# Optimization experiments

Measured on AMD Instinct MI355X. Metric: run time of the kernel, lower is better.

## Reference

```python
import jax, jax.numpy as jnp
import numpy as np

N = 50000       # nodes
E = 800000      # edges (avg degree 16)
R = 8           # relations
IN = 128        # in_channels
H = 128         # hidden_size
B = 10          # graphs in batch
NPG = N // B    # nodes per graph (equal-size graphs)
NEG_SLOPE = 0.2 # RGATConv default negative_slope


def setup_inputs() -> dict:
    key = jax.random.key(0)
    ks = jax.random.split(key, 12)
    s = 0.1
    x = jax.random.normal(ks[0], (N, IN), dtype=jnp.float32)
    edge_index = jax.random.randint(ks[1], (2, E), 0, N, dtype=jnp.int32)
    edge_type = jax.random.randint(ks[2], (E,), 0, R, dtype=jnp.int32)
    batch = jnp.repeat(jnp.arange(B, dtype=jnp.int32), NPG)
    W1 = jax.random.normal(ks[3], (R, IN, H), dtype=jnp.float32) * s
    q1 = jax.random.normal(ks[4], (H, 1), dtype=jnp.float32) * s
    k1 = jax.random.normal(ks[5], (H, 1), dtype=jnp.float32) * s
    b1 = jnp.zeros((H,), dtype=jnp.float32)
    W2 = jax.random.normal(ks[6], (R, H, H), dtype=jnp.float32) * s
    q2 = jax.random.normal(ks[7], (H, 1), dtype=jnp.float32) * s
    k2 = jax.random.normal(ks[8], (H, 1), dtype=jnp.float32) * s
    b2 = jnp.zeros((H,), dtype=jnp.float32)
    Wl = jax.random.normal(ks[9], (H, H), dtype=jnp.float32) * s
    bl = jnp.zeros((H,), dtype=jnp.float32)
    return dict(x=x, edge_index=edge_index, edge_type=edge_type, batch=batch,
                W1=W1, q1=q1, k1=k1, b1=b1, W2=W2, q2=q2, k2=k2, b2=b2,
                Wl=Wl, bl=bl)


def _rgat_conv(x, src, tgt, etype, W, q, k, b):
    # Per-relation transform once per node ([R,N,H]), then gather per edge;
    # mathematically identical to PyG's per-edge bmm but avoids the [E,in,H] blowup.
    xW = jnp.einsum('ni,rio->rno', x, W)          # [R, N, H]
    outi = xW[etype, tgt]                          # [E, H] transformed target feats
    outj = xW[etype, src]                          # [E, H] transformed source feats
    # additive self-attention, heads=1, dim=1
    alpha = jax.nn.leaky_relu(outi @ q + outj @ k, NEG_SLOPE)  # [E, 1]
    # across-relation segment softmax over incoming edges of each target node
    m = jax.ops.segment_max(alpha, tgt, num_segments=N)        # [N, 1]
    a = jnp.exp(alpha - m[tgt])
    den = jax.ops.segment_sum(a, tgt, num_segments=N)          # [N, 1]
    a = a / (den[tgt] + 1e-16)
    out = jax.ops.segment_sum(a * outj, tgt, num_segments=N)   # [N, H]
    return out + b


def reference(x, edge_index, edge_type, batch, W1, q1, k1, b1,
              W2, q2, k2, b2, Wl, bl):
    src, tgt = edge_index[0], edge_index[1]
    h = jax.nn.relu(_rgat_conv(x, src, tgt, edge_type, W1, q1, k1, b1))
    # dropout p=0 -> identity
    h = jax.nn.relu(_rgat_conv(h, src, tgt, edge_type, W2, q2, k2, b2))
    h = h @ Wl.T + bl                               # nn.Linear
    # to_dense_batch: batch is sorted with equal-size graphs of NPG nodes
    return h.reshape(B, NPG, H)
```

## Files before the change

### kernel.cpp

```cpp
#include <hip/hip_runtime.h>


typedef unsigned int uint;
typedef unsigned short ushort_t;

using bf16x8 = __attribute__((ext_vector_type(8))) __bf16;
using f32x4  = __attribute__((ext_vector_type(4))) float;

__device__ __forceinline__ ushort_t fToBf(float f) {
  uint u = __float_as_uint(f);
  u += 0x7FFFu + ((u >> 16) & 1);
  return (ushort_t)(u >> 16);
}
__device__ __forceinline__ float bfToF(ushort_t h) {
  return __uint_as_float(((uint)h) << 16);
}
__device__ __forceinline__ uint packBf(float a, float b) {
  return (uint)fToBf(a) | ((uint)fToBf(b) << 16);
}


__global__ void k_count2(const int* __restrict__ tgt, const int* __restrict__ et,
                         int* __restrict__ deg2, int E) {
  int e = blockIdx.x * 256 + threadIdx.x;
  if (e < E) atomicAdd(&deg2[tgt[e] * 8 + et[e]], 1);
}

__global__ void k_scanA(const int* __restrict__ deg, int* __restrict__ incl,
                        int* __restrict__ bsum, int n) {
  __shared__ int s[256];
  int tid = threadIdx.x;
  int i = blockIdx.x * 256 + tid;
  int v = (i < n) ? deg[i] : 0;
  s[tid] = v;
  __syncthreads();
  for (int off = 1; off < 256; off <<= 1) {
    int t = (tid >= off) ? s[tid - off] : 0;
    __syncthreads();
    s[tid] += t;
    __syncthreads();
  }
  if (i < n) incl[i] = s[tid];
  if (tid == 255) bsum[blockIdx.x] = s[255];
}

__global__ void k_scanB2(int* __restrict__ bsum, int nb) {
  __shared__ int s[256];
  __shared__ int carry;
  int tid = threadIdx.x;
  if (tid == 0) carry = 0;
  __syncthreads();
  for (int base = 0; base < nb; base += 256) {
    int i = base + tid;
    int v = (i < nb) ? bsum[i] : 0;
    s[tid] = v;
    __syncthreads();
    for (int off = 1; off < 256; off <<= 1) {
      int t = (tid >= off) ? s[tid - off] : 0;
      __syncthreads();
      s[tid] += t;
      __syncthreads();
    }
    int c = carry;
    if (i < nb) bsum[i] = c + s[tid] - v;
    __syncthreads();
    if (tid == 255) carry = c + s[255];
    __syncthreads();
  }
}

__global__ void k_scanC(const int* __restrict__ deg, const int* __restrict__ incl,
                        const int* __restrict__ bsum, int* __restrict__ rowptr,
                        int n, int E) {
  int i = blockIdx.x * 256 + threadIdx.x;
  if (i < n) {
    rowptr[i] = bsum[blockIdx.x] + incl[i] - deg[i];
    if (i == n - 1) rowptr[n] = E;
  }
}

__global__ void k_scatter2(const int* __restrict__ src, const int* __restrict__ tgt,
                           const int* __restrict__ et, const int* __restrict__ rowptr2,
                           int* __restrict__ cursor2, int* __restrict__ sorted, int E) {
  int e = blockIdx.x * 256 + threadIdx.x;
  if (e >= E) return;
  int t8r = tgt[e] * 8 + et[e];
  int pos = atomicAdd(&cursor2[t8r], 1);
  sorted[rowptr2[t8r] + pos] = src[e] | (et[e] << 16);
}


__global__ void k_wsT(const float* __restrict__ W1, const float* __restrict__ W2,
                      ushort_t* __restrict__ WsT) {
  int idx = blockIdx.x * 256 + threadIdx.x;
  int n = idx & 127;
  int k = (idx >> 7) & 127;
  int rl = idx >> 14;
  const float* W = (rl >> 3) ? W2 : W1;
  int r = rl & 7;
  float v = W[((size_t)r * 128 + k) * 128 + n];
  WsT[((size_t)rl * 128 + n) * 128 + k] = fToBf(v);
}

__global__ void k_wqwk(const float* __restrict__ W1, const float* __restrict__ q1,
                       const float* __restrict__ k1, const float* __restrict__ W2,
                       const float* __restrict__ q2, const float* __restrict__ k2,
                       ushort_t* __restrict__ wqk) {
  int g = blockIdx.x * 256 + threadIdx.x;
  if (g >= 4096) return;
  int layer = g >> 11;
  int which = (g >> 10) & 1;
  int idx = g & 1023;
  const float* w = (layer ? W2 : W1) + (size_t)idx * 128;
  const float* v = layer ? (which ? k2 : q2) : (which ? k1 : q1);
  float s = 0.f;
  #pragma unroll 8
  for (int h = 0; h < 128; h++) s += w[h] * v[h];
  int r = idx >> 7, kin = idx & 127;
  wqk[(size_t)layer * 2048 + ((which << 3) + r) * 128 + kin] = fToBf(s);
}


template <bool F32IN>
__global__ __launch_bounds__(256) void
k_score(const void* __restrict__ Ain,
        const ushort_t* __restrict__ Wqk,
        ushort_t* __restrict__ xb,
        float* __restrict__ stbl,
        int M) {
  int tid = threadIdx.x, wv = tid >> 6, lane = tid & 63;
  int l15 = lane & 15, quad = lane >> 4;
  int node0 = blockIdx.x * 128 + wv * 32;

  bf16x8 bx[2][4];
  #pragma unroll
  for (int tile = 0; tile < 2; tile++) {
    int node = node0 + tile * 16 + l15;
    int nc = node < M ? node : M - 1;
    if (F32IN) {
      const float* row = (const float*)Ain + (size_t)nc * 128;
      #pragma unroll
      for (int kb = 0; kb < 4; kb++) {
        float4 a = *(const float4*)(row + kb * 32 + quad * 8);
        float4 b = *(const float4*)(row + kb * 32 + quad * 8 + 4);
        union { bf16x8 v; ushort_t u[8]; } t;
        t.u[0] = fToBf(a.x); t.u[1] = fToBf(a.y); t.u[2] = fToBf(a.z); t.u[3] = fToBf(a.w);
        t.u[4] = fToBf(b.x); t.u[5] = fToBf(b.y); t.u[6] = fToBf(b.z); t.u[7] = fToBf(b.w);
        bx[tile][kb] = t.v;
      }
    } else {
      const ushort_t* row = (const ushort_t*)Ain + (size_t)nc * 128;
      #pragma unroll
      for (int kb = 0; kb < 4; kb++)
        bx[tile][kb] = *(const bf16x8*)(row + kb * 32 + quad * 8);
    }
  }

  if (F32IN) {
    #pragma unroll
    for (int tile = 0; tile < 2; tile++) {
      int node = node0 + tile * 16 + l15;
      if (node < M) {
        #pragma unroll
        for (int kb = 0; kb < 4; kb++)
          *(bf16x8*)(xb + (size_t)node * 128 + kb * 32 + quad * 8) = bx[tile][kb];
      }
    }
  }

  bf16x8 aq[4];
  #pragma unroll
  for (int kb = 0; kb < 4; kb++)
    aq[kb] = *(const bf16x8*)(Wqk + (size_t)l15 * 128 + kb * 32 + quad * 8);
  #pragma unroll
  for (int tile = 0; tile < 2; tile++) {
    f32x4 s = {};
    #pragma unroll
    for (int kb = 0; kb < 4; kb++)
      s = __builtin_amdgcn_mfma_f32_16x16x32_bf16(aq[kb], bx[tile][kb], s, 0, 0, 0);
    int node = node0 + tile * 16 + l15;
    if (node < M) {
      float4 v = {s[0], s[1], s[2], s[3]};
      *(float4*)(stbl + (size_t)node * 16 + quad * 4) = v;
    }
  }
}


__global__ __launch_bounds__(256) void
k_gather(const ushort_t* __restrict__ feat,
         const float* __restrict__ stbl,
         const int* __restrict__ rp2,
         const int* __restrict__ sorted,
         ushort_t* __restrict__ g,
         int n) {
  __shared__ int   s_pk[4][64];
  __shared__ float s_al[4][64];
  __shared__ float s_w[4][64];
  int tid = threadIdx.x, wv = tid >> 6, lane = tid & 63;
  int t = blockIdx.x * 4 + wv;
  if (t >= n) return;
  int e0 = rp2[t * 8], e1 = rp2[t * 8 + 8];

  float m = -INFINITY, den = 0.f;
  for (int base = e0; base < e1; base += 64) {
    int cnt = min(64, e1 - base);
    float alpha = -INFINITY;
    if (lane < cnt) {
      int pk = sorted[base + lane];
      int s = pk & 0xFFFF, r = pk >> 16;
      float a = stbl[(size_t)t * 16 + r] + stbl[(size_t)s * 16 + 8 + r];
      alpha = (a >= 0.f) ? a : 0.2f * a;
      s_pk[wv][lane] = pk;
      s_al[wv][lane] = alpha;
    }
    float cm = alpha;
    #pragma unroll
    for (int off = 32; off; off >>= 1) cm = fmaxf(cm, __shfl_xor(cm, off, 64));
    float nm = fmaxf(m, cm);
    float w = (lane < cnt) ? __expf(alpha - nm) : 0.f;
    float ws = w;
    #pragma unroll
    for (int off = 32; off; off >>= 1) ws += __shfl_xor(ws, off, 64);
    den = den * __expf(m - nm) + ws;
    m = nm;
  }
  float inv = (den > 0.f) ? 1.f / (den + 1e-16f) : 0.f;

  const uint* fx = (const uint*)feat;
  uint* grow = (uint*)(g + (size_t)t * 1024);
  float ga = 0.f, gb = 0.f;
  int rw = 0;
  bool stored = (e1 - e0) <= 64;

  for (int base = e0; base < e1; base += 64) {
    int cnt = min(64, e1 - base);
    if (lane < cnt) {
      int pk; float a;
      if (stored) {
        pk = s_pk[wv][lane];
        a = s_al[wv][lane];
      } else {
        pk = sorted[base + lane];
        int s = pk & 0xFFFF, r = pk >> 16;
        a = stbl[(size_t)t * 16 + r] + stbl[(size_t)s * 16 + 8 + r];
        a = (a >= 0.f) ? a : 0.2f * a;
        s_pk[wv][lane] = pk;
      }
      s_w[wv][lane] = __expf(a - m) * inv;
    }
    for (int i = 0; i < cnt; i++) {
      int pk = s_pk[wv][i];
      float w = s_w[wv][i];
      int r = pk >> 16;
      if (r != rw) {
        grow[rw * 64 + lane] = packBf(ga, gb);
        for (int z = rw + 1; z < r; z++) grow[z * 64 + lane] = 0u;
        rw = r; ga = 0.f; gb = 0.f;
      }
      uint v = fx[(size_t)(pk & 0xFFFF) * 64 + lane];
      ga = __builtin_fmaf(w, bfToF((ushort_t)(v & 0xFFFF)), ga);
      gb = __builtin_fmaf(w, bfToF((ushort_t)(v >> 16)), gb);
    }
  }
  grow[rw * 64 + lane] = packBf(ga, gb);
  for (int z = rw + 1; z < 8; z++) grow[z * 64 + lane] = 0u;
}


#define LDA 136

__global__ __launch_bounds__(256) void
k_out(const ushort_t* __restrict__ g,
      const ushort_t* __restrict__ WsT,
      const float* __restrict__ bias,
      ushort_t* __restrict__ h,
      int M) {
  __shared__ ushort_t As[64 * LDA];
  __shared__ ushort_t Bs[128 * LDA];
  int tid = threadIdx.x, wv = tid >> 6, lane = tid & 63;
  int l15 = lane & 15, quad = lane >> 4;
  int row0 = blockIdx.x * 64;
  int wr = wv * 16;
  f32x4 acc[8] = {};

  for (int r = 0; r < 8; r++) {
    {
      int row = tid >> 2, seg = tid & 3;
      int4 z = {0, 0, 0, 0};
      int4 v0 = z, v1 = z, v2 = z, v3 = z;
      if (row0 + row < M) {
        const int4* src = (const int4*)(g + ((size_t)(row0 + row) * 8 + r) * 128 + seg * 32);
        v0 = src[0]; v1 = src[1]; v2 = src[2]; v3 = src[3];
      }
      int4* dst = (int4*)(As + row * LDA + seg * 32);
      dst[0] = v0; dst[1] = v1; dst[2] = v2; dst[3] = v3;
    }
    {
      const int4* src = (const int4*)(WsT + (size_t)r * 16384);
      for (int u = tid; u < 512; u += 256) {
        int rowb = u >> 2, seg = u & 3;
        int4* dst = (int4*)(Bs + rowb * LDA + seg * 32);
        #pragma unroll
        for (int j = 0; j < 4; j++) dst[j] = src[rowb * 16 + seg * 4 + j];
      }
    }
    __syncthreads();

    bf16x8 afr[4];
    #pragma unroll
    for (int kb = 0; kb < 4; kb++)
      afr[kb] = *(const bf16x8*)(As + (wr + l15) * LDA + kb * 32 + quad * 8);
    #pragma unroll
    for (int ct = 0; ct < 8; ct++)
      #pragma unroll
      for (int kb = 0; kb < 4; kb++) {
        bf16x8 bfr = *(const bf16x8*)(Bs + (ct * 16 + l15) * LDA + kb * 32 + quad * 8);
        acc[ct] = __builtin_amdgcn_mfma_f32_16x16x32_bf16(afr[kb], bfr, acc[ct], 0, 0, 0);
      }
    __syncthreads();
  }

  #pragma unroll
  for (int ct = 0; ct < 8; ct++) {
    float b = bias[ct * 16 + l15];
    #pragma unroll
    for (int reg = 0; reg < 4; reg++) {
      int rr = row0 + wr + quad * 4 + reg;
      if (rr < M)
        h[(size_t)rr * 128 + ct * 16 + l15] = fToBf(fmaxf(acc[ct][reg] + b, 0.f));
    }
  }
}


__global__ __launch_bounds__(256) void
k_gemmL(const ushort_t* __restrict__ A, const float* __restrict__ Wl,
        float* __restrict__ Cout, const float* __restrict__ bias, int M) {
  __shared__ ushort_t As[64 * LDA];
  __shared__ ushort_t Bs[128 * LDA];
  int tid = threadIdx.x;
  int row0 = blockIdx.x * 64;
  for (int c = tid; c < 1024; c += 256) {
    int r = c >> 4, off = (c & 15) * 8;
    int4 v = {0, 0, 0, 0};
    if (row0 + r < M) v = *(const int4*)(A + (size_t)(row0 + r) * 128 + off);
    *(int4*)(As + r * LDA + off) = v;
  }
  for (int c = tid; c < 2048; c += 256) {
    int nn = c >> 4, off = (c & 15) * 8;
    float4 a = *(const float4*)(Wl + (size_t)nn * 128 + off);
    float4 b = *(const float4*)(Wl + (size_t)nn * 128 + off + 4);
    ushort_t* d = Bs + nn * LDA + off;
    d[0] = fToBf(a.x); d[1] = fToBf(a.y); d[2] = fToBf(a.z); d[3] = fToBf(a.w);
    d[4] = fToBf(b.x); d[5] = fToBf(b.y); d[6] = fToBf(b.z); d[7] = fToBf(b.w);
  }
  __syncthreads();
  int wv = tid >> 6, lane = tid & 63;
  int l15 = lane & 15, quad = lane >> 4;
  int wr = wv * 16;
  bf16x8 afr[4];
  #pragma unroll
  for (int kb = 0; kb < 4; kb++)
    afr[kb] = *reinterpret_cast<const bf16x8*>(As + (wr + l15) * LDA + kb * 32 + quad * 8);
  f32x4 acc[8] = {};
  #pragma unroll
  for (int ct = 0; ct < 8; ct++)
    #pragma unroll
    for (int kb = 0; kb < 4; kb++) {
      bf16x8 bfr = *reinterpret_cast<const bf16x8*>(Bs + (ct * 16 + l15) * LDA + kb * 32 + quad * 8);
      acc[ct] = __builtin_amdgcn_mfma_f32_16x16x32_bf16(afr[kb], bfr, acc[ct], 0, 0, 0);
    }
  #pragma unroll
  for (int ct = 0; ct < 8; ct++)
    #pragma unroll
    for (int reg = 0; reg < 4; reg++) {
      int rr = row0 + wr + quad * 4 + reg;
      if (rr < M) Cout[(size_t)rr * 128 + ct * 16 + l15] = acc[ct][reg] + bias[ct * 16 + l15];
    }
}


extern "C" void kernel_launch(void* const* d_in, const int* in_sizes, int n_in,
                              void* d_out, int out_size, void* d_ws, size_t ws_size,
                              hipStream_t stream) {
  const float* x   = (const float*)d_in[0];
  const int* ei    = (const int*)d_in[1];
  const int* etype = (const int*)d_in[2];
  const float* W1  = (const float*)d_in[4];
  const float* q1  = (const float*)d_in[5];
  const float* k1  = (const float*)d_in[6];
  const float* b1  = (const float*)d_in[7];
  const float* W2  = (const float*)d_in[8];
  const float* q2  = (const float*)d_in[9];
  const float* k2  = (const float*)d_in[10];
  const float* b2  = (const float*)d_in[11];
  const float* Wl  = (const float*)d_in[12];
  const float* bl  = (const float*)d_in[13];
  float* out       = (float*)d_out;

  const int N = in_sizes[0] / 128;
  const int E = in_sizes[2];

  char* ws = (char*)d_ws;
  size_t off = 0;
  auto alloc = [&](size_t bytes) {
    size_t o = off;
    off = (off + bytes + 255) & ~(size_t)255;
    return o;
  };

  ushort_t* g     = (ushort_t*)(ws + alloc((size_t)N * 1024 * 2));
  ushort_t* h1    = (ushort_t*)(ws + alloc((size_t)N * 128 * 2));
  ushort_t* xbh2  = (ushort_t*)(ws + alloc((size_t)N * 128 * 2));
  ushort_t* WsT   = (ushort_t*)(ws + alloc((size_t)2 * 8 * 16384 * 2));
  ushort_t* wqk   = (ushort_t*)(ws + alloc(2 * 16 * 128 * 2));
  float* stbl     = (float*)(ws + alloc((size_t)N * 16 * 4));
  int* deg2       = (int*)(ws + alloc((size_t)N * 8 * 4));
  int* cursor2    = (int*)(ws + alloc((size_t)N * 8 * 4));
  int* incl2      = (int*)(ws + alloc((size_t)N * 8 * 4));
  int* rowptr2    = (int*)(ws + alloc((size_t)(N * 8 + 1) * 4));
  int* bsum       = (int*)(ws + alloc(2048 * 4));
  int* sorted     = (int*)(ws + alloc((size_t)E * 4));
  (void)ws_size; (void)n_in; (void)out_size;

  const int* srcp = ei;
  const int* tgtp = ei + E;

  int n2 = N * 8;
  int gE  = (E + 255) / 256;
  int gN2 = (n2 + 255) / 256;
  int gS  = (N + 127) / 128;
  int gG  = (N + 3) / 4;
  int gO  = (N + 63) / 64;

  hipMemsetAsync(deg2, 0, (size_t)n2 * 4, stream);
  hipMemsetAsync(cursor2, 0, (size_t)n2 * 4, stream);
  k_count2<<<gE, 256, 0, stream>>>(tgtp, etype, deg2, E);
  k_scanA<<<gN2, 256, 0, stream>>>(deg2, incl2, bsum, n2);
  k_scanB2<<<1, 256, 0, stream>>>(bsum, gN2);
  k_scanC<<<gN2, 256, 0, stream>>>(deg2, incl2, bsum, rowptr2, n2, E);
  k_scatter2<<<gE, 256, 0, stream>>>(srcp, tgtp, etype, rowptr2, cursor2, sorted, E);

  k_wsT<<<1024, 256, 0, stream>>>(W1, W2, WsT);
  k_wqwk<<<16, 256, 0, stream>>>(W1, q1, k1, W2, q2, k2, wqk);

  k_score<true><<<gS, 256, 0, stream>>>(x, wqk, xbh2, stbl, N);
  k_gather<<<gG, 256, 0, stream>>>(xbh2, stbl, rowptr2, sorted, g, N);
  k_out<<<gO, 256, 0, stream>>>(g, WsT, b1, h1, N);

  k_score<false><<<gS, 256, 0, stream>>>(h1, wqk + 2048, nullptr, stbl, N);
  k_gather<<<gG, 256, 0, stream>>>(h1, stbl, rowptr2, sorted, g, N);
  k_out<<<gO, 256, 0, stream>>>(g, WsT + (size_t)8 * 16384, b2, xbh2, N);

  k_gemmL<<<gO, 256, 0, stream>>>(xbh2, Wl, out, bl, N);
}
```

Before: 476.2 us.

## Split softmax weights into separate kernel and fuse gather with per-relation GEMM

Attention weights are now computed per edge by a separate kernel and written as (source, weight) pairs. A fused kernel gathers the weighted neighbour features for each relation directly into LDS and immediately multiplies them by that relation's weight matrix. This removes the N×8×128 bf16 intermediate buffer that was written and then re-read. The GEMM B operand is now read straight from global/L2 instead of being staged in LDS. Each wave owns 16 target nodes and walks them serially, one lane per column, so the gather has lower parallelism and lower memory-level parallelism.

```diff
diff --git a/kernel.cpp b/kernel.cpp
--- a/kernel.cpp
+++ b/kernel.cpp
@@ -188,137 +188,136 @@
 
 
 __global__ __launch_bounds__(256) void
-k_gather(const ushort_t* __restrict__ feat,
-         const float* __restrict__ stbl,
-         const int* __restrict__ rp2,
-         const int* __restrict__ sorted,
-         ushort_t* __restrict__ g,
-         int n) {
-  __shared__ int   s_pk[4][64];
-  __shared__ float s_al[4][64];
-  __shared__ float s_w[4][64];
+k_weights(const float* __restrict__ stbl, const int* __restrict__ rp2,
+          const int* __restrict__ sorted, int2* __restrict__ ew, int n) {
   int tid = threadIdx.x, wv = tid >> 6, lane = tid & 63;
   int t = blockIdx.x * 4 + wv;
   if (t >= n) return;
   int e0 = rp2[t * 8], e1 = rp2[t * 8 + 8];
-
-  float m = -INFINITY, den = 0.f;
-  for (int base = e0; base < e1; base += 64) {
-    int cnt = min(64, e1 - base);
+  int deg = e1 - e0;
+  if (deg <= 0) return;
+
+  if (deg <= 64) {
     float alpha = -INFINITY;
-    if (lane < cnt) {
-      int pk = sorted[base + lane];
+    int pk = 0;
+    if (lane < deg) {
+      pk = sorted[e0 + lane];
       int s = pk & 0xFFFF, r = pk >> 16;
       float a = stbl[(size_t)t * 16 + r] + stbl[(size_t)s * 16 + 8 + r];
       alpha = (a >= 0.f) ? a : 0.2f * a;
-      s_pk[wv][lane] = pk;
-      s_al[wv][lane] = alpha;
-    }
-    float cm = alpha;
-    #pragma unroll
-    for (int off = 32; off; off >>= 1) cm = fmaxf(cm, __shfl_xor(cm, off, 64));
-    float nm = fmaxf(m, cm);
-    float w = (lane < cnt) ? __expf(alpha - nm) : 0.f;
-    float ws = w;
-    #pragma unroll
-    for (int off = 32; off; off >>= 1) ws += __shfl_xor(ws, off, 64);
-    den = den * __expf(m - nm) + ws;
-    m = nm;
-  }
-  float inv = (den > 0.f) ? 1.f / (den + 1e-16f) : 0.f;
-
-  const uint* fx = (const uint*)feat;
-  uint* grow = (uint*)(g + (size_t)t * 1024);
-  float ga = 0.f, gb = 0.f;
-  int rw = 0;
-  bool stored = (e1 - e0) <= 64;
-
-  for (int base = e0; base < e1; base += 64) {
-    int cnt = min(64, e1 - base);
-    if (lane < cnt) {
-      int pk; float a;
-      if (stored) {
-        pk = s_pk[wv][lane];
-        a = s_al[wv][lane];
-      } else {
-        pk = sorted[base + lane];
+    }
+    float m = alpha;
+    #pragma unroll
+    for (int off = 32; off; off >>= 1) m = fmaxf(m, __shfl_xor(m, off, 64));
+    float w = (lane < deg) ? __expf(alpha - m) : 0.f;
+    float den = w;
+    #pragma unroll
+    for (int off = 32; off; off >>= 1) den += __shfl_xor(den, off, 64);
+    float inv = 1.f / (den + 1e-16f);
+    if (lane < deg) {
+      int2 o;
+      o.x = pk & 0xFFFF;
+      o.y = __float_as_int(w * inv);
+      ew[e0 + lane] = o;
+    }
+  } else {
+    float m = -INFINITY, den = 0.f;
+    for (int base = e0; base < e1; base += 64) {
+      int cnt = min(64, e1 - base);
+      float alpha = -INFINITY;
+      if (lane < cnt) {
+        int pk = sorted[base + lane];
         int s = pk & 0xFFFF, r = pk >> 16;
-        a = stbl[(size_t)t * 16 + r] + stbl[(size_t)s * 16 + 8 + r];
+        float a = stbl[(size_t)t * 16 + r] + stbl[(size_t)s * 16 + 8 + r];
+        alpha = (a >= 0.f) ? a : 0.2f * a;
+      }
+      float cm = alpha;
+      #pragma unroll
+      for (int off = 32; off; off >>= 1) cm = fmaxf(cm, __shfl_xor(cm, off, 64));
+      float nm = fmaxf(m, cm);
+      float w = (lane < cnt) ? __expf(alpha - nm) : 0.f;
+      float ws = w;
+      #pragma unroll
+      for (int off = 32; off; off >>= 1) ws += __shfl_xor(ws, off, 64);
+      den = den * __expf(m - nm) + ws;
+      m = nm;
+    }
+    float inv = 1.f / (den + 1e-16f);
+    for (int base = e0; base < e1; base += 64) {
+      int cnt = min(64, e1 - base);
+      if (lane < cnt) {
+        int pk = sorted[base + lane];
+        int s = pk & 0xFFFF, r = pk >> 16;
+        float a = stbl[(size_t)t * 16 + r] + stbl[(size_t)s * 16 + 8 + r];
         a = (a >= 0.f) ? a : 0.2f * a;
-        s_pk[wv][lane] = pk;
-      }
-      s_w[wv][lane] = __expf(a - m) * inv;
-    }
-    for (int i = 0; i < cnt; i++) {
-      int pk = s_pk[wv][i];
-      float w = s_w[wv][i];
-      int r = pk >> 16;
-      if (r != rw) {
-        grow[rw * 64 + lane] = packBf(ga, gb);
-        for (int z = rw + 1; z < r; z++) grow[z * 64 + lane] = 0u;
-        rw = r; ga = 0.f; gb = 0.f;
-      }
-      uint v = fx[(size_t)(pk & 0xFFFF) * 64 + lane];
-      ga = __builtin_fmaf(w, bfToF((ushort_t)(v & 0xFFFF)), ga);
-      gb = __builtin_fmaf(w, bfToF((ushort_t)(v >> 16)), gb);
-    }
-  }
-  grow[rw * 64 + lane] = packBf(ga, gb);
-  for (int z = rw + 1; z < 8; z++) grow[z * 64 + lane] = 0u;
+        int2 o;
+        o.x = pk & 0xFFFF;
+        o.y = __float_as_int(__expf(a - m) * inv);
+        ew[base + lane] = o;
+      }
+    }
+  }
 }
 
 
 #define LDA 136
 
-__global__ __launch_bounds__(256) void
-k_out(const ushort_t* __restrict__ g,
-      const ushort_t* __restrict__ WsT,
-      const float* __restrict__ bias,
-      ushort_t* __restrict__ h,
-      int M) {
-  __shared__ ushort_t As[64 * LDA];
-  __shared__ ushort_t Bs[128 * LDA];
+__global__ __launch_bounds__(256, 4) void
+k_fused(const ushort_t* __restrict__ feat,
+        const int* __restrict__ rp2,
+        const int2* __restrict__ ew,
+        const ushort_t* __restrict__ WsT,
+        const float* __restrict__ bias,
+        ushort_t* __restrict__ h,
+        int M) {
+  __shared__ __align__(16) ushort_t As[64 * LDA];
   int tid = threadIdx.x, wv = tid >> 6, lane = tid & 63;
   int l15 = lane & 15, quad = lane >> 4;
-  int row0 = blockIdx.x * 64;
-  int wr = wv * 16;
+  int t0 = blockIdx.x * 64 + wv * 16;
+  const uint* fx = (const uint*)feat;
+  uint* asu = (uint*)As;
   f32x4 acc[8] = {};
 
   for (int r = 0; r < 8; r++) {
-    {
-      int row = tid >> 2, seg = tid & 3;
-      int4 z = {0, 0, 0, 0};
-      int4 v0 = z, v1 = z, v2 = z, v3 = z;
-      if (row0 + row < M) {
-        const int4* src = (const int4*)(g + ((size_t)(row0 + row) * 8 + r) * 128 + seg * 32);
-        v0 = src[0]; v1 = src[1]; v2 = src[2]; v3 = src[3];
-      }
-      int4* dst = (int4*)(As + row * LDA + seg * 32);
-      dst[0] = v0; dst[1] = v1; dst[2] = v2; dst[3] = v3;
-    }
-    {
-      const int4* src = (const int4*)(WsT + (size_t)r * 16384);
-      for (int u = tid; u < 512; u += 256) {
-        int rowb = u >> 2, seg = u & 3;
-        int4* dst = (int4*)(Bs + rowb * LDA + seg * 32);
-        #pragma unroll
-        for (int j = 0; j < 4; j++) dst[j] = src[rowb * 16 + seg * 4 + j];
-      }
-    }
-    __syncthreads();
-
+    for (int i = 0; i < 16; i++) {
+      int t = t0 + i;
+      float ga = 0.f, gb = 0.f;
+      if (t < M) {
+        int e = rp2[t * 8 + r], eend = rp2[t * 8 + r + 1];
+        for (; e + 1 < eend; e += 2) {
+          int2 p0 = ew[e];
+          int2 p1 = ew[e + 1];
+          uint v0 = fx[(size_t)p0.x * 64 + lane];
+          uint v1 = fx[(size_t)p1.x * 64 + lane];
+          float w0 = __int_as_float(p0.y);
+          float w1 = __int_as_float(p1.y);
+          ga = __builtin_fmaf(w0, bfToF((ushort_t)(v0 & 0xFFFF)), ga);
+          gb = __builtin_fmaf(w0, bfToF((ushort_t)(v0 >> 16)), gb);
+          ga = __builtin_fmaf(w1, bfToF((ushort_t)(v1 & 0xFFFF)), ga);
+          gb = __builtin_fmaf(w1, bfToF((ushort_t)(v1 >> 16)), gb);
+        }
+        if (e < eend) {
+          int2 p = ew[e];
+          uint v = fx[(size_t)p.x * 64 + lane];
+          float w = __int_as_float(p.y);
+          ga = __builtin_fmaf(w, bfToF((ushort_t)(v & 0xFFFF)), ga);
+          gb = __builtin_fmaf(w, bfToF((ushort_t)(v >> 16)), gb);
+        }
+      }
+      asu[(wv * 16 + i) * (LDA / 2) + lane] = packBf(ga, gb);
+    }
     bf16x8 afr[4];
     #pragma unroll
     for (int kb = 0; kb < 4; kb++)
-      afr[kb] = *(const bf16x8*)(As + (wr + l15) * LDA + kb * 32 + quad * 8);
+      afr[kb] = *(const bf16x8*)(As + (size_t)(wv * 16 + l15) * LDA + kb * 32 + quad * 8);
+    const ushort_t* Wr = WsT + (size_t)r * 16384;
     #pragma unroll
     for (int ct = 0; ct < 8; ct++)
       #pragma unroll
       for (int kb = 0; kb < 4; kb++) {
-        bf16x8 bfr = *(const bf16x8*)(Bs + (ct * 16 + l15) * LDA + kb * 32 + quad * 8);
+        bf16x8 bfr = *(const bf16x8*)(Wr + (size_t)(ct * 16 + l15) * 128 + kb * 32 + quad * 8);
         acc[ct] = __builtin_amdgcn_mfma_f32_16x16x32_bf16(afr[kb], bfr, acc[ct], 0, 0, 0);
       }
-    __syncthreads();
   }
 
   #pragma unroll
@@ -326,7 +325,7 @@
     float b = bias[ct * 16 + l15];
     #pragma unroll
     for (int reg = 0; reg < 4; reg++) {
-      int rr = row0 + wr + quad * 4 + reg;
+      int rr = t0 + quad * 4 + reg;
       if (rr < M)
         h[(size_t)rr * 128 + ct * 16 + l15] = fToBf(fmaxf(acc[ct][reg] + b, 0.f));
     }
@@ -410,12 +409,12 @@
     return o;
   };
 
-  ushort_t* g     = (ushort_t*)(ws + alloc((size_t)N * 1024 * 2));
   ushort_t* h1    = (ushort_t*)(ws + alloc((size_t)N * 128 * 2));
   ushort_t* xbh2  = (ushort_t*)(ws + alloc((size_t)N * 128 * 2));
   ushort_t* WsT   = (ushort_t*)(ws + alloc((size_t)2 * 8 * 16384 * 2));
   ushort_t* wqk   = (ushort_t*)(ws + alloc(2 * 16 * 128 * 2));
   float* stbl     = (float*)(ws + alloc((size_t)N * 16 * 4));
+  int2* ew        = (int2*)(ws + alloc((size_t)E * 8));
   int* deg2       = (int*)(ws + alloc((size_t)N * 8 * 4));
   int* cursor2    = (int*)(ws + alloc((size_t)N * 8 * 4));
   int* incl2      = (int*)(ws + alloc((size_t)N * 8 * 4));
@@ -431,8 +430,8 @@
   int gE  = (E + 255) / 256;
   int gN2 = (n2 + 255) / 256;
   int gS  = (N + 127) / 128;
-  int gG  = (N + 3) / 4;
-  int gO  = (N + 63) / 64;
+  int gW  = (N + 3) / 4;
+  int gF  = (N + 63) / 64;
 
   hipMemsetAsync(deg2, 0, (size_t)n2 * 4, stream);
   hipMemsetAsync(cursor2, 0, (size_t)n2 * 4, stream);
@@ -446,12 +445,12 @@
   k_wqwk<<<16, 256, 0, stream>>>(W1, q1, k1, W2, q2, k2, wqk);
 
   k_score<true><<<gS, 256, 0, stream>>>(x, wqk, xbh2, stbl, N);
-  k_gather<<<gG, 256, 0, stream>>>(xbh2, stbl, rowptr2, sorted, g, N);
-  k_out<<<gO, 256, 0, stream>>>(g, WsT, b1, h1, N);
+  k_weights<<<gW, 256, 0, stream>>>(stbl, rowptr2, sorted, ew, N);
+  k_fused<<<gF, 256, 0, stream>>>(xbh2, rowptr2, ew, WsT, b1, h1, N);
 
   k_score<false><<<gS, 256, 0, stream>>>(h1, wqk + 2048, nullptr, stbl, N);
-  k_gather<<<gG, 256, 0, stream>>>(h1, stbl, rowptr2, sorted, g, N);
-  k_out<<<gO, 256, 0, stream>>>(g, WsT + (size_t)8 * 16384, b2, xbh2, N);
-
-  k_gemmL<<<gO, 256, 0, stream>>>(xbh2, Wl, out, bl, N);
-}
+  k_weights<<<gW, 256, 0, stream>>>(stbl, rowptr2, sorted, ew, N);
+  k_fused<<<gF, 256, 0, stream>>>(h1, rowptr2, ew, WsT + (size_t)8 * 16384, b2, xbh2, N);
+
+  k_gemmL<<<gF, 256, 0, stream>>>(xbh2, Wl, out, bl, N);
+}
```

Measured after the change: 714.5 us. 50.0% more time.

## Gather four edges per wave with 16-byte loads into LDS accumulators

Applied to the files above, without the earlier changes.

The per-target gather now processes four edges at once per wave, each 16-lane group loading a full 256-byte source row with uint4 loads and accumulating into a per-wave LDS buffer for the eight relations. The old version did one edge per iteration with 4-byte loads. The softmax has a single-pass fast path for degree at most 64. The cursor is also seeded with the row pointer, which removes a memset and one indirection in the scatter, and the two weight-prep kernels are merged into one launch. The LDS read-modify-write accumulation is serialized across the four groups, which adds LDS traffic and a larger shared-memory footprint.

```diff
diff --git a/kernel.cpp b/kernel.cpp
--- a/kernel.cpp
+++ b/kernel.cpp
@@ -71,53 +71,54 @@
 
 __global__ void k_scanC(const int* __restrict__ deg, const int* __restrict__ incl,
                         const int* __restrict__ bsum, int* __restrict__ rowptr,
-                        int n, int E) {
+                        int* __restrict__ cur, int n, int E) {
   int i = blockIdx.x * 256 + threadIdx.x;
   if (i < n) {
-    rowptr[i] = bsum[blockIdx.x] + incl[i] - deg[i];
+    int v = bsum[blockIdx.x] + incl[i] - deg[i];
+    rowptr[i] = v;
+    cur[i] = v;
     if (i == n - 1) rowptr[n] = E;
   }
 }
 
 __global__ void k_scatter2(const int* __restrict__ src, const int* __restrict__ tgt,
-                           const int* __restrict__ et, const int* __restrict__ rowptr2,
-                           int* __restrict__ cursor2, int* __restrict__ sorted, int E) {
+                           const int* __restrict__ et, int* __restrict__ cur,
+                           int* __restrict__ sorted, int E) {
   int e = blockIdx.x * 256 + threadIdx.x;
   if (e >= E) return;
   int t8r = tgt[e] * 8 + et[e];
-  int pos = atomicAdd(&cursor2[t8r], 1);
-  sorted[rowptr2[t8r] + pos] = src[e] | (et[e] << 16);
-}
-
-
-__global__ void k_wsT(const float* __restrict__ W1, const float* __restrict__ W2,
-                      ushort_t* __restrict__ WsT) {
-  int idx = blockIdx.x * 256 + threadIdx.x;
-  int n = idx & 127;
-  int k = (idx >> 7) & 127;
-  int rl = idx >> 14;
-  const float* W = (rl >> 3) ? W2 : W1;
-  int r = rl & 7;
-  float v = W[((size_t)r * 128 + k) * 128 + n];
-  WsT[((size_t)rl * 128 + n) * 128 + k] = fToBf(v);
-}
-
-__global__ void k_wqwk(const float* __restrict__ W1, const float* __restrict__ q1,
+  int pos = atomicAdd(&cur[t8r], 1);
+  sorted[pos] = src[e] | (et[e] << 16);
+}
+
+
+__global__ void k_prep(const float* __restrict__ W1, const float* __restrict__ q1,
                        const float* __restrict__ k1, const float* __restrict__ W2,
                        const float* __restrict__ q2, const float* __restrict__ k2,
-                       ushort_t* __restrict__ wqk) {
-  int g = blockIdx.x * 256 + threadIdx.x;
-  if (g >= 4096) return;
-  int layer = g >> 11;
-  int which = (g >> 10) & 1;
-  int idx = g & 1023;
-  const float* w = (layer ? W2 : W1) + (size_t)idx * 128;
-  const float* v = layer ? (which ? k2 : q2) : (which ? k1 : q1);
-  float s = 0.f;
-  #pragma unroll 8
-  for (int h = 0; h < 128; h++) s += w[h] * v[h];
-  int r = idx >> 7, kin = idx & 127;
-  wqk[(size_t)layer * 2048 + ((which << 3) + r) * 128 + kin] = fToBf(s);
+                       ushort_t* __restrict__ WsT, ushort_t* __restrict__ wqk) {
+  int b = blockIdx.x;
+  if (b < 1024) {
+    int idx = b * 256 + threadIdx.x;
+    int n = idx & 127;
+    int k = (idx >> 7) & 127;
+    int rl = idx >> 14;
+    const float* W = (rl >> 3) ? W2 : W1;
+    int r = rl & 7;
+    float v = W[((size_t)r * 128 + k) * 128 + n];
+    WsT[((size_t)rl * 128 + n) * 128 + k] = fToBf(v);
+  } else {
+    int g = (b - 1024) * 256 + threadIdx.x;
+    int layer = g >> 11;
+    int which = (g >> 10) & 1;
+    int idx = g & 1023;
+    const float* w = (layer ? W2 : W1) + (size_t)idx * 128;
+    const float* v = layer ? (which ? k2 : q2) : (which ? k1 : q1);
+    float s = 0.f;
+    #pragma unroll 8
+    for (int hh = 0; hh < 128; hh++) s += w[hh] * v[hh];
+    int r = idx >> 7, kin = idx & 127;
+    wqk[(size_t)layer * 2048 + ((which << 3) + r) * 128 + kin] = fToBf(s);
+  }
 }
 
 
@@ -188,83 +189,121 @@
 
 
 __global__ __launch_bounds__(256) void
-k_gather(const ushort_t* __restrict__ feat,
-         const float* __restrict__ stbl,
-         const int* __restrict__ rp2,
-         const int* __restrict__ sorted,
-         ushort_t* __restrict__ g,
-         int n) {
+k_gather2(const ushort_t* __restrict__ feat,
+          const float* __restrict__ stbl,
+          const int* __restrict__ rp2,
+          const int* __restrict__ sorted,
+          ushort_t* __restrict__ g,
+          int n) {
+  __shared__ float gacc[4][8 * 132];
   __shared__ int   s_pk[4][64];
-  __shared__ float s_al[4][64];
   __shared__ float s_w[4][64];
   int tid = threadIdx.x, wv = tid >> 6, lane = tid & 63;
+  int g4 = lane >> 4, fcol = lane & 15;
   int t = blockIdx.x * 4 + wv;
   if (t >= n) return;
+
+  float* gw = gacc[wv];
+  for (int i = lane; i < 1056; i += 64) gw[i] = 0.f;
+
   int e0 = rp2[t * 8], e1 = rp2[t * 8 + 8];
-
-  float m = -INFINITY, den = 0.f;
-  for (int base = e0; base < e1; base += 64) {
-    int cnt = min(64, e1 - base);
+  int deg = e1 - e0;
+  float m = -INFINITY, inv = 0.f;
+  bool fast = (deg <= 64);
+
+  if (fast) {
     float alpha = -INFINITY;
-    if (lane < cnt) {
-      int pk = sorted[base + lane];
+    int pk = 0;
+    if (lane < deg) {
+      pk = sorted[e0 + lane];
       int s = pk & 0xFFFF, r = pk >> 16;
       float a = stbl[(size_t)t * 16 + r] + stbl[(size_t)s * 16 + 8 + r];
       alpha = (a >= 0.f) ? a : 0.2f * a;
-      s_pk[wv][lane] = pk;
-      s_al[wv][lane] = alpha;
-    }
-    float cm = alpha;
-    #pragma unroll
-    for (int off = 32; off; off >>= 1) cm = fmaxf(cm, __shfl_xor(cm, off, 64));
-    float nm = fmaxf(m, cm);
-    float w = (lane < cnt) ? __expf(alpha - nm) : 0.f;
-    float ws = w;
-    #pragma unroll
-    for (int off = 32; off; off >>= 1) ws += __shfl_xor(ws, off, 64);
-    den = den * __expf(m - nm) + ws;
-    m = nm;
-  }
-  float inv = (den > 0.f) ? 1.f / (den + 1e-16f) : 0.f;
-
-  const uint* fx = (const uint*)feat;
-  uint* grow = (uint*)(g + (size_t)t * 1024);
-  float ga = 0.f, gb = 0.f;
-  int rw = 0;
-  bool stored = (e1 - e0) <= 64;
-
-  for (int base = e0; base < e1; base += 64) {
-    int cnt = min(64, e1 - base);
-    if (lane < cnt) {
-      int pk; float a;
-      if (stored) {
-        pk = s_pk[wv][lane];
-        a = s_al[wv][lane];
-      } else {
-        pk = sorted[base + lane];
+    }
+    m = alpha;
+    #pragma unroll
+    for (int off = 32; off; off >>= 1) m = fmaxf(m, __shfl_xor(m, off, 64));
+    float w = (lane < deg) ? __expf(alpha - m) : 0.f;
+    float den = w;
+    #pragma unroll
+    for (int off = 32; off; off >>= 1) den += __shfl_xor(den, off, 64);
+    inv = 1.f / (den + 1e-16f);
+    s_pk[wv][lane] = (lane < deg) ? pk : 0;
+    s_w[wv][lane] = w * inv;
+  } else {
+    float den = 0.f;
+    for (int base = e0; base < e1; base += 64) {
+      int cnt = min(64, e1 - base);
+      float alpha = -INFINITY;
+      if (lane < cnt) {
+        int pk = sorted[base + lane];
         int s = pk & 0xFFFF, r = pk >> 16;
-        a = stbl[(size_t)t * 16 + r] + stbl[(size_t)s * 16 + 8 + r];
-        a = (a >= 0.f) ? a : 0.2f * a;
-        s_pk[wv][lane] = pk;
-      }
-      s_w[wv][lane] = __expf(a - m) * inv;
-    }
-    for (int i = 0; i < cnt; i++) {
-      int pk = s_pk[wv][i];
-      float w = s_w[wv][i];
-      int r = pk >> 16;
-      if (r != rw) {
-        grow[rw * 64 + lane] = packBf(ga, gb);
-        for (int z = rw + 1; z < r; z++) grow[z * 64 + lane] = 0u;
-        rw = r; ga = 0.f; gb = 0.f;
-      }
-      uint v = fx[(size_t)(pk & 0xFFFF) * 64 + lane];
-      ga = __builtin_fmaf(w, bfToF((ushort_t)(v & 0xFFFF)), ga);
-      gb = __builtin_fmaf(w, bfToF((ushort_t)(v >> 16)), gb);
-    }
-  }
-  grow[rw * 64 + lane] = packBf(ga, gb);
-  for (int z = rw + 1; z < 8; z++) grow[z * 64 + lane] = 0u;
+        float a = stbl[(size_t)t * 16 + r] + stbl[(size_t)s * 16 + 8 + r];
+        alpha = (a >= 0.f) ? a : 0.2f * a;
+      }
+      float cm = alpha;
+      #pragma unroll
+      for (int off = 32; off; off >>= 1) cm = fmaxf(cm, __shfl_xor(cm, off, 64));
+      float nm = fmaxf(m, cm);
+      float w = (lane < cnt) ? __expf(alpha - nm) : 0.f;
+      float ws = w;
+      #pragma unroll
+      for (int off = 32; off; off >>= 1) ws += __shfl_xor(ws, off, 64);
+      den = den * __expf(m - nm) + ws;
+      m = nm;
+    }
+    inv = 1.f / (den + 1e-16f);
+  }
+
+  const uint4* fx4 = (const uint4*)feat;
+  for (int base = e0; base < e1; base += 4) {
+    int i = base + g4;
+    bool valid = (i < e1);
+    int pk = 0;
+    float w = 0.f;
+    if (fast) {
+      int li = i - e0;
+      if (valid) {
+        pk = s_pk[wv][li];
+        w = s_w[wv][li];
+      }
+    } else if (valid) {
+      pk = sorted[i];
+      int s = pk & 0xFFFF, r = pk >> 16;
+      float a = stbl[(size_t)t * 16 + r] + stbl[(size_t)s * 16 + 8 + r];
+      a = (a >= 0.f) ? a : 0.2f * a;
+      w = __expf(a - m) * inv;
+    }
+    int src = pk & 0xFFFF, r = pk >> 16;
+    uint4 v = {0, 0, 0, 0};
+    if (valid) v = fx4[(size_t)src * 16 + fcol];
+    float* row = gw + r * 132 + fcol * 8;
+    #pragma unroll
+    for (int s4 = 0; s4 < 4; s4++) {
+      if (g4 == s4 && valid) {
+        float4 c0 = *(float4*)row;
+        float4 c1 = *(float4*)(row + 4);
+        c0.x = __builtin_fmaf(w, bfToF((ushort_t)(v.x & 0xFFFF)), c0.x);
+        c0.y = __builtin_fmaf(w, bfToF((ushort_t)(v.x >> 16)),    c0.y);
+        c0.z = __builtin_fmaf(w, bfToF((ushort_t)(v.y & 0xFFFF)), c0.z);
+        c0.w = __builtin_fmaf(w, bfToF((ushort_t)(v.y >> 16)),    c0.w);
+        c1.x = __builtin_fmaf(w, bfToF((ushort_t)(v.z & 0xFFFF)), c1.x);
+        c1.y = __builtin_fmaf(w, bfToF((ushort_t)(v.z >> 16)),    c1.y);
+        c1.z = __builtin_fmaf(w, bfToF((ushort_t)(v.w & 0xFFFF)), c1.z);
+        c1.w = __builtin_fmaf(w, bfToF((ushort_t)(v.w >> 16)),    c1.w);
+        *(float4*)row = c0;
+        *(float4*)(row + 4) = c1;
+      }
+    }
+  }
+
+  uint* gout = (uint*)(g + (size_t)t * 1024);
+  #pragma unroll
+  for (int r = 0; r < 8; r++) {
+    float a = gw[r * 132 + lane * 2];
+    float b = gw[r * 132 + lane * 2 + 1];
+    gout[r * 64 + lane] = packBf(a, b);
+  }
 }
 
 
@@ -417,7 +456,7 @@
   ushort_t* wqk   = (ushort_t*)(ws + alloc(2 * 16 * 128 * 2));
   float* stbl     = (float*)(ws + alloc((size_t)N * 16 * 4));
   int* deg2       = (int*)(ws + alloc((size_t)N * 8 * 4));
-  int* cursor2    = (int*)(ws + alloc((size_t)N * 8 * 4));
+  int* cur2       = (int*)(ws + alloc((size_t)N * 8 * 4));
   int* incl2      = (int*)(ws + alloc((size_t)N * 8 * 4));
   int* rowptr2    = (int*)(ws + alloc((size_t)(N * 8 + 1) * 4));
   int* bsum       = (int*)(ws + alloc(2048 * 4));
@@ -435,22 +474,20 @@
   int gO  = (N + 63) / 64;
 
   hipMemsetAsync(deg2, 0, (size_t)n2 * 4, stream);
-  hipMemsetAsync(cursor2, 0, (size_t)n2 * 4, stream);
   k_count2<<<gE, 256, 0, stream>>>(tgtp, etype, deg2, E);
   k_scanA<<<gN2, 256, 0, stream>>>(deg2, incl2, bsum, n2);
   k_scanB2<<<1, 256, 0, stream>>>(bsum, gN2);
-  k_scanC<<<gN2, 256, 0, stream>>>(deg2, incl2, bsum, rowptr2, n2, E);
-  k_scatter2<<<gE, 256, 0, stream>>>(srcp, tgtp, etype, rowptr2, cursor2, sorted, E);
-
-  k_wsT<<<1024, 256, 0, stream>>>(W1, W2, WsT);
-  k_wqwk<<<16, 256, 0, stream>>>(W1, q1, k1, W2, q2, k2, wqk);
+  k_scanC<<<gN2, 256, 0, stream>>>(deg2, incl2, bsum, rowptr2, cur2, n2, E);
+  k_scatter2<<<gE, 256, 0, stream>>>(srcp, tgtp, etype, cur2, sorted, E);
+
+  k_prep<<<1040, 256, 0, stream>>>(W1, q1, k1, W2, q2, k2, WsT, wqk);
 
   k_score<true><<<gS, 256, 0, stream>>>(x, wqk, xbh2, stbl, N);
-  k_gather<<<gG, 256, 0, stream>>>(xbh2, stbl, rowptr2, sorted, g, N);
+  k_gather2<<<gG, 256, 0, stream>>>(xbh2, stbl, rowptr2, sorted, g, N);
   k_out<<<gO, 256, 0, stream>>>(g, WsT, b1, h1, N);
 
   k_score<false><<<gS, 256, 0, stream>>>(h1, wqk + 2048, nullptr, stbl, N);
-  k_gather<<<gG, 256, 0, stream>>>(h1, stbl, rowptr2, sorted, g, N);
+  k_gather2<<<gG, 256, 0, stream>>>(h1, stbl, rowptr2, sorted, g, N);
   k_out<<<gO, 256, 0, stream>>>(g, WsT + (size_t)8 * 16384, b2, xbh2, N);
 
   k_gemmL<<<gO, 256, 0, stream>>>(xbh2, Wl, out, bl, N);
```

After: 479.7 us. About the same (+0.7%).
